# Optimization experiments

Measured on AMD Instinct MI355X. Metric: run time of the kernel, lower is better.

Reference implementation:

```python
import jax, jax.numpy as jnp
import numpy as np

H = 4  # num_heads


def _ln(x, g, b, eps=1e-5):
    m = x.mean(-1, keepdims=True)
    v = ((x - m) ** 2).mean(-1, keepdims=True)
    return (x - m) / jnp.sqrt(v + eps) * g + b


def setup_inputs() -> dict:
    key = jax.random.key(0)
    ks = jax.random.split(key, 16)
    B, N, M, dQ, dK, dV = 4, 2048, 2048, 128, 128, 128
    s = 0.02
    return {
        "Q": jax.random.normal(ks[0], (B, N, dQ), jnp.float32),
        "K": jax.random.normal(ks[1], (B, M, dK), jnp.float32),
        "adj_mask": jax.random.randint(ks[2], (B, N, M), 0, 2, jnp.int32),
        "Wq": jax.random.normal(ks[3], (dQ, dV), jnp.float32) * s,
        "bq": jnp.zeros((dV,), jnp.float32),
        "Wk": jax.random.normal(ks[4], (dK, dV), jnp.float32) * s,
        "bk": jnp.zeros((dV,), jnp.float32),
        "Wv": jax.random.normal(ks[5], (dK, dV), jnp.float32) * s,
        "bv": jnp.zeros((dV,), jnp.float32),
        "Wr1": jax.random.normal(ks[6], (dV, dV), jnp.float32) * s,
        "br1": jnp.zeros((dV,), jnp.float32),
        "Wr2": jax.random.normal(ks[7], (dV, dV), jnp.float32) * s,
        "br2": jnp.zeros((dV,), jnp.float32),
        "g0": jnp.ones((dV,), jnp.float32),
        "be0": jnp.zeros((dV,), jnp.float32),
        "g1": jnp.ones((dV,), jnp.float32),
        "be1": jnp.zeros((dV,), jnp.float32),
    }


def reference(Q, K, adj_mask, Wq, bq, Wk, bk, Wv, bv, Wr1, br1, Wr2, br2, g0, be0, g1, be1):
    B, N, _ = Q.shape
    M = K.shape[1]
    dV = Wq.shape[1]
    dh = dV // H
    Qp = Q @ Wq + bq   # [B,N,dV]
    Kp = K @ Wk + bk   # [B,M,dV]
    Vp = K @ Wv + bv   # [B,M,dV]
    # torch: split dim_V into H chunks, cat along dim 0 -> head-major [H*B, L, dh]
    def to_heads(x, L):
        return x.reshape(B, L, H, dh).transpose(2, 0, 1, 3).reshape(H * B, L, dh)
    Qh, Kh, Vh = to_heads(Qp, N), to_heads(Kp, M), to_heads(Vp, M)
    attn = jnp.einsum('bnd,bmd->bnm', Qh, Kh) / jnp.sqrt(jnp.float32(dh))  # [H*B,N,M]
    # torch repeat_interleave(mask, H, dim=0) gives batch-major order -- faithful
    mask = jnp.repeat(adj_mask, H, axis=0)
    attn = jnp.where(mask == 0, -jnp.inf, attn)
    A = jax.nn.softmax(attn, axis=2)
    O = Qh + jnp.einsum('bnm,bmd->bnd', A, Vh)  # [H*B,N,dh]
    # recombine heads back to [B,N,dV] (intended split(dim=0)/cat(dim=2))
    O = O.reshape(H, B, N, dh).transpose(1, 2, 0, 3).reshape(B, N, dV)
    O = _ln(O, g0, be0)
    O = O + (jax.nn.relu(O @ Wr1 + br1) @ Wr2 + br2)
    return _ln(O, g1, be1)
```

## Files before the change

### kernel.cpp

```cpp
#include <hip/hip_runtime.h>
#include <hip/hip_bf16.h>


typedef short bf16x8 __attribute__((ext_vector_type(8)));
typedef float f32x4 __attribute__((ext_vector_type(4)));

#define BN 4
#define SEQ 2048
#define DIM 128
#define NH 4
#define DH 32
#define ROWS (BN * SEQ)
#define MS 4

static __device__ __forceinline__ unsigned short f2bf(float f) {
    __hip_bfloat16 h = __float2bfloat16(f);
    return *reinterpret_cast<unsigned short*>(&h);
}

__global__ __launch_bounds__(256) void prep_weights(
    const float* __restrict__ Wq, const float* __restrict__ Wk,
    const float* __restrict__ Wv, const float* __restrict__ W1,
    const float* __restrict__ W2, unsigned short* __restrict__ WT)
{
    const float* Ws[5] = {Wq, Wk, Wv, W1, W2};
    const float* W = Ws[blockIdx.x];
    unsigned short* out = WT + blockIdx.x * DIM * DIM;
    for (int i = threadIdx.x; i < DIM * DIM; i += 256) {
        int n = i >> 7, k = i & 127;
        out[i] = f2bf(W[k * DIM + n]);
    }
}

__global__ __launch_bounds__(256) void proj_kernel(
    const float* __restrict__ Q, const float* __restrict__ K,
    const float* __restrict__ bq, const float* __restrict__ bk,
    const float* __restrict__ bv, const unsigned short* __restrict__ WT,
    float* __restrict__ Qp, unsigned short* __restrict__ Qb,
    unsigned short* __restrict__ Kb, unsigned short* __restrict__ Vt)
{
    __shared__ __align__(16) unsigned short sX[64][136];
    __shared__ __align__(16) unsigned short sY[64][137];

    const int proj = blockIdx.y;
    const int rowbase = blockIdx.x * 64;
    const float* X = (proj == 0) ? Q : K;
    const unsigned short* Wt = WT + proj * DIM * DIM;
    const float* bias = (proj == 0) ? bq : (proj == 1) ? bk : bv;

    const int t = threadIdx.x;
    for (int i = 0; i < 8; ++i) {
        int idx = i * 256 + t;
        int row = idx >> 5, c4 = (idx & 31) * 4;
        float4 v = *(const float4*)(X + (rowbase + row) * DIM + c4);
        sX[row][c4 + 0] = f2bf(v.x);
        sX[row][c4 + 1] = f2bf(v.y);
        sX[row][c4 + 2] = f2bf(v.z);
        sX[row][c4 + 3] = f2bf(v.w);
    }
    __syncthreads();

    const int w = t >> 6, lane = t & 63;
    const int n16 = lane & 15, quad = lane >> 4;

    f32x4 acc[4][2];
    for (int r = 0; r < 4; ++r)
        for (int ct = 0; ct < 2; ++ct)
            acc[r][ct] = (f32x4){0.f, 0.f, 0.f, 0.f};

    for (int ks = 0; ks < 4; ++ks) {
        bf16x8 bfrag[2];
        for (int ct = 0; ct < 2; ++ct) {
            int ncol = w * 32 + ct * 16 + n16;
            bfrag[ct] = *(const bf16x8*)(Wt + ncol * DIM + ks * 32 + quad * 8);
        }
        for (int r = 0; r < 4; ++r) {
            bf16x8 afrag = *(const bf16x8*)(&sX[r * 16 + n16][ks * 32 + quad * 8]);
            for (int ct = 0; ct < 2; ++ct)
                acc[r][ct] = __builtin_amdgcn_mfma_f32_16x16x32_bf16(
                    afrag, bfrag[ct], acc[r][ct], 0, 0, 0);
        }
    }

    for (int r = 0; r < 4; ++r) {
        for (int ct = 0; ct < 2; ++ct) {
            int col = w * 32 + ct * 16 + n16;
            float bv_ = bias[col];
            for (int i = 0; i < 4; ++i) {
                int lrow = r * 16 + quad * 4 + i;
                int grow = rowbase + lrow;
                float val = acc[r][ct][i] + bv_;
                if (proj == 0) {
                    Qp[grow * DIM + col] = val;
                    Qb[grow * DIM + col] = f2bf(val * 0.17677669529663687f);
                } else if (proj == 1) {
                    Kb[grow * DIM + col] = f2bf(val);
                } else {
                    sY[lrow][col] = f2bf(val);
                }
            }
        }
    }
    if (proj == 2) {
        __syncthreads();
        int b = rowbase >> 11;
        int mm0 = rowbase & 2047;
        for (int i = 0; i < 32; ++i) {
            int idx = i * 256 + t;
            int c = idx >> 6, m = idx & 63;
            Vt[(b * DIM + c) * SEQ + mm0 + m] = sY[m][c];
        }
    }
}

__global__ __launch_bounds__(256) void attn_kernel(
    const unsigned short* __restrict__ Qb, const unsigned short* __restrict__ Kb,
    const unsigned short* __restrict__ Vt, const int* __restrict__ adj,
    float* __restrict__ Opart, float* __restrict__ Lpart)
{
    __shared__ __align__(16) unsigned short sP[4][16][68];

    const int h = blockIdx.y;
    const int qbase = blockIdx.x * 32;
    const int sp = blockIdx.z;
    const int t = threadIdx.x;
    const int b = t >> 6;
    const int lane = t & 63, n16 = lane & 15, quad = lane >> 4;

    bf16x8 qfrag[2];
#pragma unroll
    for (int r = 0; r < 2; ++r)
        qfrag[r] = *(const bf16x8*)(Qb + ((long)b * SEQ + qbase + r * 16 + n16) * DIM
                                       + h * DH + quad * 8);

    const unsigned short* Kp = Kb + (long)b * SEQ * DIM + h * DH + quad * 8;
    const unsigned short* Vp = Vt + (long)(b * DIM + h * DH) * SEQ + quad * 8;
    const int* Mp = adj + (long)h * SEQ * SEQ + n16;

    int mrow[8];
#pragma unroll
    for (int r = 0; r < 2; ++r)
#pragma unroll
        for (int i = 0; i < 4; ++i)
            mrow[r * 4 + i] = (qbase + r * 16 + quad * 4 + i) * SEQ;

    f32x4 o[2][2];
    float lsum[2][4];
#pragma unroll
    for (int r = 0; r < 2; ++r) {
#pragma unroll
        for (int ct = 0; ct < 2; ++ct) o[r][ct] = (f32x4){0.f, 0.f, 0.f, 0.f};
#pragma unroll
        for (int i = 0; i < 4; ++i) lsum[r][i] = 0.f;
    }

    bf16x8 kf[2][2], vf[2][2];
    int mk[2][16];
    const int mb0 = sp * 512;

#pragma unroll
    for (int c = 0; c < 2; ++c) {
        kf[0][c] = *(const bf16x8*)(Kp + (long)(mb0 + c * 16 + n16) * DIM);
        vf[0][c] = *(const bf16x8*)(Vp + (long)(c * 16 + n16) * SEQ + mb0);
    }
#pragma unroll
    for (int j = 0; j < 8; ++j) {
        mk[0][j]     = Mp[mrow[j] + mb0];
        mk[0][8 + j] = Mp[mrow[j] + mb0 + 16];
    }

    const f32x4 zero4 = {0.f, 0.f, 0.f, 0.f};

#pragma unroll
    for (int mt = 0; mt < 16; ++mt) {
        const int cur = mt & 1, nxt = cur ^ 1;
        if (mt < 15) {
            const int mb = mb0 + (mt + 1) * 32;
#pragma unroll
            for (int c = 0; c < 2; ++c) {
                kf[nxt][c] = *(const bf16x8*)(Kp + (long)(mb + c * 16 + n16) * DIM);
                vf[nxt][c] = *(const bf16x8*)(Vp + (long)(c * 16 + n16) * SEQ + mb);
            }
#pragma unroll
            for (int j = 0; j < 8; ++j) {
                mk[nxt][j]     = Mp[mrow[j] + mb];
                mk[nxt][8 + j] = Mp[mrow[j] + mb + 16];
            }
        }
#pragma unroll
        for (int r = 0; r < 2; ++r) {
            f32x4 s0 = __builtin_amdgcn_mfma_f32_16x16x32_bf16(qfrag[r], kf[cur][0], zero4, 0, 0, 0);
            f32x4 s1 = __builtin_amdgcn_mfma_f32_16x16x32_bf16(qfrag[r], kf[cur][1], zero4, 0, 0, 0);
#pragma unroll
            for (int i = 0; i < 4; ++i) {
                float p0 = mk[cur][r * 4 + i]     ? __expf(s0[i]) : 0.f;
                float p1 = mk[cur][8 + r * 4 + i] ? __expf(s1[i]) : 0.f;
                lsum[r][i] += p0 + p1;
                sP[b][quad * 4 + i][n16]      = f2bf(p0);
                sP[b][quad * 4 + i][16 + n16] = f2bf(p1);
            }
            bf16x8 pa = *(const bf16x8*)(&sP[b][n16][quad * 8]);
#pragma unroll
            for (int ct = 0; ct < 2; ++ct)
                o[r][ct] = __builtin_amdgcn_mfma_f32_16x16x32_bf16(pa, vf[cur][ct], o[r][ct], 0, 0, 0);
        }
    }

#pragma unroll
    for (int d = 1; d < 16; d <<= 1)
#pragma unroll
        for (int r = 0; r < 2; ++r)
#pragma unroll
            for (int i = 0; i < 4; ++i)
                lsum[r][i] += __shfl_xor(lsum[r][i], d, 64);

    float* Ob = Opart + ((long)sp * ROWS + (long)b * SEQ) * DIM;
#pragma unroll
    for (int r = 0; r < 2; ++r)
#pragma unroll
        for (int ct = 0; ct < 2; ++ct)
#pragma unroll
            for (int i = 0; i < 4; ++i)
                Ob[(qbase + r * 16 + quad * 4 + i) * DIM + h * DH + ct * 16 + n16] = o[r][ct][i];

    if (n16 == 0) {
#pragma unroll
        for (int r = 0; r < 2; ++r)
#pragma unroll
            for (int i = 0; i < 4; ++i)
                Lpart[(((long)sp * BN + b) * NH + h) * SEQ + qbase + r * 16 + quad * 4 + i]
                    = lsum[r][i];
    }
}

__global__ __launch_bounds__(256) void epi_kernel(
    const float* __restrict__ Qp, const float* __restrict__ Opart,
    const float* __restrict__ Lpart, const unsigned short* __restrict__ WT,
    const float* __restrict__ br1, const float* __restrict__ br2,
    const float* __restrict__ g0, const float* __restrict__ be0,
    const float* __restrict__ g1, const float* __restrict__ be1,
    float* __restrict__ out)
{
    __shared__ __align__(16) unsigned short sXb[32][136];
    __shared__ __align__(16) unsigned short sHb[32][136];
    __shared__ __align__(16) float sXf[32][132];

    const int rowbase = blockIdx.x * 32;
    const int t = threadIdx.x;
    const int row = t >> 3, c16 = (t & 7) * 16;
    const int grow = rowbase + row;
    const int bidx = grow >> 11;
    const int srow = grow & 2047;
    const int head = c16 >> 5;

    {
        float l = 0.f;
#pragma unroll
        for (int s = 0; s < MS; ++s)
            l += Lpart[(((long)s * BN + bidx) * NH + head) * SEQ + srow];
        float linv = 1.f / l;

        float vals[16];
        float sum = 0.f, ss = 0.f;
#pragma unroll
        for (int j = 0; j < 16; j += 4) {
            float4 qv = *(const float4*)(Qp + (long)grow * DIM + c16 + j);
            float4 ov = {0.f, 0.f, 0.f, 0.f};
#pragma unroll
            for (int s = 0; s < MS; ++s) {
                float4 p = *(const float4*)(Opart + ((long)s * ROWS + grow) * DIM + c16 + j);
                ov.x += p.x; ov.y += p.y; ov.z += p.z; ov.w += p.w;
            }
            vals[j + 0] = qv.x + ov.x * linv;
            vals[j + 1] = qv.y + ov.y * linv;
            vals[j + 2] = qv.z + ov.z * linv;
            vals[j + 3] = qv.w + ov.w * linv;
#pragma unroll
            for (int u = 0; u < 4; ++u) { sum += vals[j + u]; ss += vals[j + u] * vals[j + u]; }
        }
        sum += __shfl_xor(sum, 1, 64); sum += __shfl_xor(sum, 2, 64); sum += __shfl_xor(sum, 4, 64);
        ss  += __shfl_xor(ss, 1, 64);  ss  += __shfl_xor(ss, 2, 64);  ss  += __shfl_xor(ss, 4, 64);
        float mean = sum * (1.f / 128.f);
        float var  = ss * (1.f / 128.f) - mean * mean;
        float rstd = rsqrtf(var + 1e-5f);
#pragma unroll
        for (int j = 0; j < 16; ++j) {
            int col = c16 + j;
            float x = (vals[j] - mean) * rstd * g0[col] + be0[col];
            sXf[row][col] = x;
            sXb[row][col] = f2bf(x);
        }
    }
    __syncthreads();

    const int w = t >> 6, lane = t & 63;
    const int n16 = lane & 15, quad = lane >> 4;
    const unsigned short* W1t = WT + 3 * DIM * DIM;
    const unsigned short* W2t = WT + 4 * DIM * DIM;

    f32x4 acc[2][2];
#pragma unroll
    for (int r = 0; r < 2; ++r)
#pragma unroll
        for (int ct = 0; ct < 2; ++ct) acc[r][ct] = (f32x4){0.f, 0.f, 0.f, 0.f};
    for (int ks = 0; ks < 4; ++ks) {
        bf16x8 bfrag[2];
#pragma unroll
        for (int ct = 0; ct < 2; ++ct)
            bfrag[ct] = *(const bf16x8*)(W1t + (w * 32 + ct * 16 + n16) * DIM + ks * 32 + quad * 8);
#pragma unroll
        for (int r = 0; r < 2; ++r) {
            bf16x8 afrag = *(const bf16x8*)(&sXb[r * 16 + n16][ks * 32 + quad * 8]);
#pragma unroll
            for (int ct = 0; ct < 2; ++ct)
                acc[r][ct] = __builtin_amdgcn_mfma_f32_16x16x32_bf16(
                    afrag, bfrag[ct], acc[r][ct], 0, 0, 0);
        }
    }
#pragma unroll
    for (int r = 0; r < 2; ++r)
#pragma unroll
        for (int ct = 0; ct < 2; ++ct) {
            int col = w * 32 + ct * 16 + n16;
            float bb = br1[col];
#pragma unroll
            for (int i = 0; i < 4; ++i) {
                float hv = acc[r][ct][i] + bb;
                sHb[r * 16 + quad * 4 + i][col] = f2bf(fmaxf(hv, 0.f));
            }
        }
    __syncthreads();

    f32x4 acc2[2][2];
#pragma unroll
    for (int r = 0; r < 2; ++r)
#pragma unroll
        for (int ct = 0; ct < 2; ++ct) acc2[r][ct] = (f32x4){0.f, 0.f, 0.f, 0.f};
    for (int ks = 0; ks < 4; ++ks) {
        bf16x8 bfrag[2];
#pragma unroll
        for (int ct = 0; ct < 2; ++ct)
            bfrag[ct] = *(const bf16x8*)(W2t + (w * 32 + ct * 16 + n16) * DIM + ks * 32 + quad * 8);
#pragma unroll
        for (int r = 0; r < 2; ++r) {
            bf16x8 afrag = *(const bf16x8*)(&sHb[r * 16 + n16][ks * 32 + quad * 8]);
#pragma unroll
            for (int ct = 0; ct < 2; ++ct)
                acc2[r][ct] = __builtin_amdgcn_mfma_f32_16x16x32_bf16(
                    afrag, bfrag[ct], acc2[r][ct], 0, 0, 0);
        }
    }
    float yv[2][2][4];
#pragma unroll
    for (int r = 0; r < 2; ++r)
#pragma unroll
        for (int ct = 0; ct < 2; ++ct) {
            int col = w * 32 + ct * 16 + n16;
            float bb = br2[col];
#pragma unroll
            for (int i = 0; i < 4; ++i)
                yv[r][ct][i] = acc2[r][ct][i] + bb + sXf[r * 16 + quad * 4 + i][col];
        }
    __syncthreads();
#pragma unroll
    for (int r = 0; r < 2; ++r)
#pragma unroll
        for (int ct = 0; ct < 2; ++ct) {
            int col = w * 32 + ct * 16 + n16;
#pragma unroll
            for (int i = 0; i < 4; ++i)
                sXf[r * 16 + quad * 4 + i][col] = yv[r][ct][i];
        }
    __syncthreads();

    {
        float vals[16];
        float sum = 0.f, ss = 0.f;
#pragma unroll
        for (int j = 0; j < 16; ++j) {
            float v = sXf[row][c16 + j];
            vals[j] = v; sum += v; ss += v * v;
        }
        sum += __shfl_xor(sum, 1, 64); sum += __shfl_xor(sum, 2, 64); sum += __shfl_xor(sum, 4, 64);
        ss  += __shfl_xor(ss, 1, 64);  ss  += __shfl_xor(ss, 2, 64);  ss  += __shfl_xor(ss, 4, 64);
        float mean = sum * (1.f / 128.f);
        float var  = ss * (1.f / 128.f) - mean * mean;
        float rstd = rsqrtf(var + 1e-5f);
        float* op = out + (long)grow * DIM + c16;
#pragma unroll
        for (int j = 0; j < 16; j += 4) {
            float4 ov;
            int col = c16 + j;
            ov.x = (vals[j + 0] - mean) * rstd * g1[col + 0] + be1[col + 0];
            ov.y = (vals[j + 1] - mean) * rstd * g1[col + 1] + be1[col + 1];
            ov.z = (vals[j + 2] - mean) * rstd * g1[col + 2] + be1[col + 2];
            ov.w = (vals[j + 3] - mean) * rstd * g1[col + 3] + be1[col + 3];
            *(float4*)(op + j) = ov;
        }
    }
}

extern "C" void kernel_launch(void* const* d_in, const int* in_sizes, int n_in,
                              void* d_out, int out_size, void* d_ws, size_t ws_size,
                              hipStream_t stream) {
    const float* Q   = (const float*)d_in[0];
    const float* K   = (const float*)d_in[1];
    const int*   adj = (const int*)d_in[2];
    const float* Wq  = (const float*)d_in[3];
    const float* bq  = (const float*)d_in[4];
    const float* Wk  = (const float*)d_in[5];
    const float* bk  = (const float*)d_in[6];
    const float* Wv  = (const float*)d_in[7];
    const float* bv  = (const float*)d_in[8];
    const float* Wr1 = (const float*)d_in[9];
    const float* br1 = (const float*)d_in[10];
    const float* Wr2 = (const float*)d_in[11];
    const float* br2 = (const float*)d_in[12];
    const float* g0  = (const float*)d_in[13];
    const float* be0 = (const float*)d_in[14];
    const float* g1  = (const float*)d_in[15];
    const float* be1 = (const float*)d_in[16];
    float* out = (float*)d_out;

    float* Qp          = (float*)d_ws;
    float* Opart       = Qp + (long)ROWS * DIM;
    float* Lpart       = Opart + (long)MS * ROWS * DIM;
    unsigned short* Qb = (unsigned short*)(Lpart + (long)MS * BN * NH * SEQ);
    unsigned short* Kb = Qb + (long)ROWS * DIM;
    unsigned short* Vt = Kb + (long)ROWS * DIM;
    unsigned short* WT = Vt + (long)ROWS * DIM;

    prep_weights<<<5, 256, 0, stream>>>(Wq, Wk, Wv, Wr1, Wr2, WT);
    proj_kernel<<<dim3(128, 3), 256, 0, stream>>>(Q, K, bq, bk, bv, WT,
                                                  Qp, Qb, Kb, Vt);
    attn_kernel<<<dim3(64, NH, MS), 256, 0, stream>>>(Qb, Kb, Vt, adj, Opart, Lpart);
    epi_kernel<<<256, 256, 0, stream>>>(Qp, Opart, Lpart, WT, br1, br2,
                                        g0, be0, g1, be1, out);
}
```

Measured before the change: 188.6 us.

## Bit-pack adjacency mask, store bf16 partial outputs, shrink proj/epilogue tiles

A new prep kernel packs the int32 adjacency mask into 32-bit words before the attention kernel runs, so attention reads one bit per key instead of a full int32. Partial attention outputs are now stored as bf16 instead of fp32, which halves the traffic between the attention and epilogue kernels at some cost in precision. The projection and epilogue kernels use half the rows per block to launch more blocks. The attention inner loop is also reordered so all four QK MFMAs issue before the softmax and P writes.

```diff
diff --git a/kernel.cpp b/kernel.cpp
--- a/kernel.cpp
+++ b/kernel.cpp
@@ -12,24 +12,48 @@
 #define DH 32
 #define ROWS (BN * SEQ)
 #define MS 4
+#define MWORDS (SEQ / 32)
 
 static __device__ __forceinline__ unsigned short f2bf(float f) {
     __hip_bfloat16 h = __float2bfloat16(f);
     return *reinterpret_cast<unsigned short*>(&h);
 }
-
-__global__ __launch_bounds__(256) void prep_weights(
+static __device__ __forceinline__ float bf2f(unsigned short u) {
+    union { unsigned int i; float f; } cv;
+    cv.i = ((unsigned int)u) << 16;
+    return cv.f;
+}
+
+__global__ __launch_bounds__(256) void pack_prep(
+    const int* __restrict__ adj,
     const float* __restrict__ Wq, const float* __restrict__ Wk,
     const float* __restrict__ Wv, const float* __restrict__ W1,
-    const float* __restrict__ W2, unsigned short* __restrict__ WT)
+    const float* __restrict__ W2,
+    unsigned int* __restrict__ bits, unsigned short* __restrict__ WT)
 {
-    const float* Ws[5] = {Wq, Wk, Wv, W1, W2};
-    const float* W = Ws[blockIdx.x];
-    unsigned short* out = WT + blockIdx.x * DIM * DIM;
-    for (int i = threadIdx.x; i < DIM * DIM; i += 256) {
-        int n = i >> 7, k = i & 127;
-        out[i] = f2bf(W[k * DIM + n]);
-    }
+    const int bx = blockIdx.x;
+    if (bx >= 2048) {
+        const float* Ws[5] = {Wq, Wk, Wv, W1, W2};
+        const float* W = Ws[bx - 2048];
+        unsigned short* out = WT + (bx - 2048) * DIM * DIM;
+        for (int i = threadIdx.x; i < DIM * DIM; i += 256) {
+            int n = i >> 7, k = i & 127;
+            out[i] = f2bf(W[k * DIM + n]);
+        }
+        return;
+    }
+    const int wid = bx * 256 + threadIdx.x;
+    const int4* src = (const int4*)(adj + (long)wid * 32);
+    unsigned int w = 0;
+#pragma unroll
+    for (int j = 0; j < 8; ++j) {
+        int4 v = src[j];
+        w |= (((unsigned)v.x & 1u) << (4 * j))
+           | (((unsigned)v.y & 1u) << (4 * j + 1))
+           | (((unsigned)v.z & 1u) << (4 * j + 2))
+           | (((unsigned)v.w & 1u) << (4 * j + 3));
+    }
+    bits[wid] = w;
 }
 
 __global__ __launch_bounds__(256) void proj_kernel(
@@ -39,20 +63,21 @@
     float* __restrict__ Qp, unsigned short* __restrict__ Qb,
     unsigned short* __restrict__ Kb, unsigned short* __restrict__ Vt)
 {
-    __shared__ __align__(16) unsigned short sX[64][136];
-    __shared__ __align__(16) unsigned short sY[64][137];
+    __shared__ __align__(16) unsigned short sX[32][136];
+    __shared__ __align__(16) unsigned short sY[32][137];
 
     const int proj = blockIdx.y;
-    const int rowbase = blockIdx.x * 64;
+    const int rowbase = blockIdx.x * 32;
     const float* X = (proj == 0) ? Q : K;
     const unsigned short* Wt = WT + proj * DIM * DIM;
     const float* bias = (proj == 0) ? bq : (proj == 1) ? bk : bv;
 
     const int t = threadIdx.x;
-    for (int i = 0; i < 8; ++i) {
+#pragma unroll
+    for (int i = 0; i < 4; ++i) {
         int idx = i * 256 + t;
         int row = idx >> 5, c4 = (idx & 31) * 4;
-        float4 v = *(const float4*)(X + (rowbase + row) * DIM + c4);
+        float4 v = *(const float4*)(X + (long)(rowbase + row) * DIM + c4);
         sX[row][c4 + 0] = f2bf(v.x);
         sX[row][c4 + 1] = f2bf(v.y);
         sX[row][c4 + 2] = f2bf(v.z);
@@ -63,38 +88,46 @@
     const int w = t >> 6, lane = t & 63;
     const int n16 = lane & 15, quad = lane >> 4;
 
-    f32x4 acc[4][2];
-    for (int r = 0; r < 4; ++r)
+    f32x4 acc[2][2];
+#pragma unroll
+    for (int r = 0; r < 2; ++r)
+#pragma unroll
         for (int ct = 0; ct < 2; ++ct)
             acc[r][ct] = (f32x4){0.f, 0.f, 0.f, 0.f};
 
     for (int ks = 0; ks < 4; ++ks) {
         bf16x8 bfrag[2];
+#pragma unroll
         for (int ct = 0; ct < 2; ++ct) {
             int ncol = w * 32 + ct * 16 + n16;
             bfrag[ct] = *(const bf16x8*)(Wt + ncol * DIM + ks * 32 + quad * 8);
         }
-        for (int r = 0; r < 4; ++r) {
+#pragma unroll
+        for (int r = 0; r < 2; ++r) {
             bf16x8 afrag = *(const bf16x8*)(&sX[r * 16 + n16][ks * 32 + quad * 8]);
+#pragma unroll
             for (int ct = 0; ct < 2; ++ct)
                 acc[r][ct] = __builtin_amdgcn_mfma_f32_16x16x32_bf16(
                     afrag, bfrag[ct], acc[r][ct], 0, 0, 0);
         }
     }
 
-    for (int r = 0; r < 4; ++r) {
+#pragma unroll
+    for (int r = 0; r < 2; ++r) {
+#pragma unroll
         for (int ct = 0; ct < 2; ++ct) {
             int col = w * 32 + ct * 16 + n16;
             float bv_ = bias[col];
+#pragma unroll
             for (int i = 0; i < 4; ++i) {
                 int lrow = r * 16 + quad * 4 + i;
                 int grow = rowbase + lrow;
                 float val = acc[r][ct][i] + bv_;
                 if (proj == 0) {
-                    Qp[grow * DIM + col] = val;
-                    Qb[grow * DIM + col] = f2bf(val * 0.17677669529663687f);
+                    Qp[(long)grow * DIM + col] = val;
+                    Qb[(long)grow * DIM + col] = f2bf(val * 0.17677669529663687f);
                 } else if (proj == 1) {
-                    Kb[grow * DIM + col] = f2bf(val);
+                    Kb[(long)grow * DIM + col] = f2bf(val);
                 } else {
                     sY[lrow][col] = f2bf(val);
                 }
@@ -105,20 +138,21 @@
         __syncthreads();
         int b = rowbase >> 11;
         int mm0 = rowbase & 2047;
-        for (int i = 0; i < 32; ++i) {
+#pragma unroll
+        for (int i = 0; i < 16; ++i) {
             int idx = i * 256 + t;
-            int c = idx >> 6, m = idx & 63;
-            Vt[(b * DIM + c) * SEQ + mm0 + m] = sY[m][c];
+            int c = idx >> 5, m = idx & 31;
+            Vt[((long)b * DIM + c) * SEQ + mm0 + m] = sY[m][c];
         }
     }
 }
 
 __global__ __launch_bounds__(256) void attn_kernel(
     const unsigned short* __restrict__ Qb, const unsigned short* __restrict__ Kb,
-    const unsigned short* __restrict__ Vt, const int* __restrict__ adj,
-    float* __restrict__ Opart, float* __restrict__ Lpart)
+    const unsigned short* __restrict__ Vt, const unsigned int* __restrict__ mbits,
+    unsigned short* __restrict__ Opart, float* __restrict__ Lpart)
 {
-    __shared__ __align__(16) unsigned short sP[4][16][68];
+    __shared__ __align__(16) unsigned short sP[4][32][68];
 
     const int h = blockIdx.y;
     const int qbase = blockIdx.x * 32;
@@ -135,14 +169,14 @@
 
     const unsigned short* Kp = Kb + (long)b * SEQ * DIM + h * DH + quad * 8;
     const unsigned short* Vp = Vt + (long)(b * DIM + h * DH) * SEQ + quad * 8;
-    const int* Mp = adj + (long)h * SEQ * SEQ + n16;
-
-    int mrow[8];
+
+    int mrowb[8];
 #pragma unroll
     for (int r = 0; r < 2; ++r)
 #pragma unroll
         for (int i = 0; i < 4; ++i)
-            mrow[r * 4 + i] = (qbase + r * 16 + quad * 4 + i) * SEQ;
+            mrowb[r * 4 + i] = (h * SEQ + qbase + r * 16 + quad * 4 + i) * MWORDS
+                             + sp * 16;
 
     f32x4 o[2][2];
     float lsum[2][4];
@@ -155,7 +189,7 @@
     }
 
     bf16x8 kf[2][2], vf[2][2];
-    int mk[2][16];
+    unsigned int mk[2][8];
     const int mb0 = sp * 512;
 
 #pragma unroll
@@ -164,10 +198,7 @@
         vf[0][c] = *(const bf16x8*)(Vp + (long)(c * 16 + n16) * SEQ + mb0);
     }
 #pragma unroll
-    for (int j = 0; j < 8; ++j) {
-        mk[0][j]     = Mp[mrow[j] + mb0];
-        mk[0][8 + j] = Mp[mrow[j] + mb0 + 16];
-    }
+    for (int j = 0; j < 8; ++j) mk[0][j] = mbits[mrowb[j]];
 
     const f32x4 zero4 = {0.f, 0.f, 0.f, 0.f};
 
@@ -182,27 +213,33 @@
                 vf[nxt][c] = *(const bf16x8*)(Vp + (long)(c * 16 + n16) * SEQ + mb);
             }
 #pragma unroll
-            for (int j = 0; j < 8; ++j) {
-                mk[nxt][j]     = Mp[mrow[j] + mb];
-                mk[nxt][8 + j] = Mp[mrow[j] + mb + 16];
+            for (int j = 0; j < 8; ++j) mk[nxt][j] = mbits[mrowb[j] + mt + 1];
+        }
+        f32x4 s[2][2];
+#pragma unroll
+        for (int r = 0; r < 2; ++r)
+#pragma unroll
+            for (int c = 0; c < 2; ++c)
+                s[r][c] = __builtin_amdgcn_mfma_f32_16x16x32_bf16(
+                    qfrag[r], kf[cur][c], zero4, 0, 0, 0);
+#pragma unroll
+        for (int r = 0; r < 2; ++r)
+#pragma unroll
+            for (int i = 0; i < 4; ++i) {
+                unsigned int w = mk[cur][r * 4 + i];
+                float p0 = ((w >> n16) & 1u)        ? __expf(s[r][0][i]) : 0.f;
+                float p1 = ((w >> (16 + n16)) & 1u) ? __expf(s[r][1][i]) : 0.f;
+                lsum[r][i] += p0 + p1;
+                sP[b][r * 16 + quad * 4 + i][n16]      = f2bf(p0);
+                sP[b][r * 16 + quad * 4 + i][16 + n16] = f2bf(p1);
             }
-        }
 #pragma unroll
         for (int r = 0; r < 2; ++r) {
-            f32x4 s0 = __builtin_amdgcn_mfma_f32_16x16x32_bf16(qfrag[r], kf[cur][0], zero4, 0, 0, 0);
-            f32x4 s1 = __builtin_amdgcn_mfma_f32_16x16x32_bf16(qfrag[r], kf[cur][1], zero4, 0, 0, 0);
-#pragma unroll
-            for (int i = 0; i < 4; ++i) {
-                float p0 = mk[cur][r * 4 + i]     ? __expf(s0[i]) : 0.f;
-                float p1 = mk[cur][8 + r * 4 + i] ? __expf(s1[i]) : 0.f;
-                lsum[r][i] += p0 + p1;
-                sP[b][quad * 4 + i][n16]      = f2bf(p0);
-                sP[b][quad * 4 + i][16 + n16] = f2bf(p1);
-            }
-            bf16x8 pa = *(const bf16x8*)(&sP[b][n16][quad * 8]);
+            bf16x8 pa = *(const bf16x8*)(&sP[b][r * 16 + n16][quad * 8]);
 #pragma unroll
             for (int ct = 0; ct < 2; ++ct)
-                o[r][ct] = __builtin_amdgcn_mfma_f32_16x16x32_bf16(pa, vf[cur][ct], o[r][ct], 0, 0, 0);
+                o[r][ct] = __builtin_amdgcn_mfma_f32_16x16x32_bf16(
+                    pa, vf[cur][ct], o[r][ct], 0, 0, 0);
         }
     }
 
@@ -214,14 +251,15 @@
             for (int i = 0; i < 4; ++i)
                 lsum[r][i] += __shfl_xor(lsum[r][i], d, 64);
 
-    float* Ob = Opart + ((long)sp * ROWS + (long)b * SEQ) * DIM;
+    unsigned short* Ob = Opart + ((long)sp * ROWS + (long)b * SEQ) * DIM;
 #pragma unroll
     for (int r = 0; r < 2; ++r)
 #pragma unroll
         for (int ct = 0; ct < 2; ++ct)
 #pragma unroll
             for (int i = 0; i < 4; ++i)
-                Ob[(qbase + r * 16 + quad * 4 + i) * DIM + h * DH + ct * 16 + n16] = o[r][ct][i];
+                Ob[(long)(qbase + r * 16 + quad * 4 + i) * DIM + h * DH + ct * 16 + n16]
+                    = f2bf(o[r][ct][i]);
 
     if (n16 == 0) {
 #pragma unroll
@@ -234,24 +272,24 @@
 }
 
 __global__ __launch_bounds__(256) void epi_kernel(
-    const float* __restrict__ Qp, const float* __restrict__ Opart,
+    const float* __restrict__ Qp, const unsigned short* __restrict__ Opart,
     const float* __restrict__ Lpart, const unsigned short* __restrict__ WT,
     const float* __restrict__ br1, const float* __restrict__ br2,
     const float* __restrict__ g0, const float* __restrict__ be0,
     const float* __restrict__ g1, const float* __restrict__ be1,
     float* __restrict__ out)
 {
-    __shared__ __align__(16) unsigned short sXb[32][136];
-    __shared__ __align__(16) unsigned short sHb[32][136];
-    __shared__ __align__(16) float sXf[32][132];
-
-    const int rowbase = blockIdx.x * 32;
+    __shared__ __align__(16) unsigned short sXb[16][136];
+    __shared__ __align__(16) unsigned short sHb[16][136];
+    __shared__ __align__(16) float sXf[16][132];
+
+    const int rowbase = blockIdx.x * 16;
     const int t = threadIdx.x;
-    const int row = t >> 3, c16 = (t & 7) * 16;
+    const int row = t >> 4, col8 = (t & 15) * 8;
     const int grow = rowbase + row;
     const int bidx = grow >> 11;
     const int srow = grow & 2047;
-    const int head = c16 >> 5;
+    const int head = col8 >> 5;
 
     {
         float l = 0.f;
@@ -260,32 +298,38 @@
             l += Lpart[(((long)s * BN + bidx) * NH + head) * SEQ + srow];
         float linv = 1.f / l;
 
-        float vals[16];
+        float ovf[8];
+#pragma unroll
+        for (int j = 0; j < 8; ++j) ovf[j] = 0.f;
+#pragma unroll
+        for (int s = 0; s < MS; ++s) {
+            bf16x8 p = *(const bf16x8*)(Opart + ((long)s * ROWS + grow) * DIM + col8);
+#pragma unroll
+            for (int j = 0; j < 8; ++j) ovf[j] += bf2f((unsigned short)p[j]);
+        }
+
+        float vals[8];
         float sum = 0.f, ss = 0.f;
 #pragma unroll
-        for (int j = 0; j < 16; j += 4) {
-            float4 qv = *(const float4*)(Qp + (long)grow * DIM + c16 + j);
-            float4 ov = {0.f, 0.f, 0.f, 0.f};
-#pragma unroll
-            for (int s = 0; s < MS; ++s) {
-                float4 p = *(const float4*)(Opart + ((long)s * ROWS + grow) * DIM + c16 + j);
-                ov.x += p.x; ov.y += p.y; ov.z += p.z; ov.w += p.w;
-            }
-            vals[j + 0] = qv.x + ov.x * linv;
-            vals[j + 1] = qv.y + ov.y * linv;
-            vals[j + 2] = qv.z + ov.z * linv;
-            vals[j + 3] = qv.w + ov.w * linv;
+        for (int j = 0; j < 8; j += 4) {
+            float4 qv = *(const float4*)(Qp + (long)grow * DIM + col8 + j);
+            vals[j + 0] = qv.x + ovf[j + 0] * linv;
+            vals[j + 1] = qv.y + ovf[j + 1] * linv;
+            vals[j + 2] = qv.z + ovf[j + 2] * linv;
+            vals[j + 3] = qv.w + ovf[j + 3] * linv;
 #pragma unroll
             for (int u = 0; u < 4; ++u) { sum += vals[j + u]; ss += vals[j + u] * vals[j + u]; }
         }
-        sum += __shfl_xor(sum, 1, 64); sum += __shfl_xor(sum, 2, 64); sum += __shfl_xor(sum, 4, 64);
-        ss  += __shfl_xor(ss, 1, 64);  ss  += __shfl_xor(ss, 2, 64);  ss  += __shfl_xor(ss, 4, 64);
+        sum += __shfl_xor(sum, 1, 64); sum += __shfl_xor(sum, 2, 64);
+        sum += __shfl_xor(sum, 4, 64); sum += __shfl_xor(sum, 8, 64);
+        ss  += __shfl_xor(ss, 1, 64);  ss  += __shfl_xor(ss, 2, 64);
+        ss  += __shfl_xor(ss, 4, 64);  ss  += __shfl_xor(ss, 8, 64);
         float mean = sum * (1.f / 128.f);
         float var  = ss * (1.f / 128.f) - mean * mean;
         float rstd = rsqrtf(var + 1e-5f);
 #pragma unroll
-        for (int j = 0; j < 16; ++j) {
-            int col = c16 + j;
+        for (int j = 0; j < 8; ++j) {
+            int col = col8 + j;
             float x = (vals[j] - mean) * rstd * g0[col] + be0[col];
             sXf[row][col] = x;
             sXb[row][col] = f2bf(x);
@@ -298,99 +342,79 @@
     const unsigned short* W1t = WT + 3 * DIM * DIM;
     const unsigned short* W2t = WT + 4 * DIM * DIM;
 
-    f32x4 acc[2][2];
-#pragma unroll
-    for (int r = 0; r < 2; ++r)
-#pragma unroll
-        for (int ct = 0; ct < 2; ++ct) acc[r][ct] = (f32x4){0.f, 0.f, 0.f, 0.f};
+    f32x4 acc[2];
+#pragma unroll
+    for (int ct = 0; ct < 2; ++ct) acc[ct] = (f32x4){0.f, 0.f, 0.f, 0.f};
     for (int ks = 0; ks < 4; ++ks) {
-        bf16x8 bfrag[2];
-#pragma unroll
-        for (int ct = 0; ct < 2; ++ct)
-            bfrag[ct] = *(const bf16x8*)(W1t + (w * 32 + ct * 16 + n16) * DIM + ks * 32 + quad * 8);
-#pragma unroll
-        for (int r = 0; r < 2; ++r) {
-            bf16x8 afrag = *(const bf16x8*)(&sXb[r * 16 + n16][ks * 32 + quad * 8]);
-#pragma unroll
-            for (int ct = 0; ct < 2; ++ct)
-                acc[r][ct] = __builtin_amdgcn_mfma_f32_16x16x32_bf16(
-                    afrag, bfrag[ct], acc[r][ct], 0, 0, 0);
-        }
-    }
-#pragma unroll
-    for (int r = 0; r < 2; ++r)
+        bf16x8 afrag = *(const bf16x8*)(&sXb[n16][ks * 32 + quad * 8]);
 #pragma unroll
         for (int ct = 0; ct < 2; ++ct) {
-            int col = w * 32 + ct * 16 + n16;
-            float bb = br1[col];
-#pragma unroll
-            for (int i = 0; i < 4; ++i) {
-                float hv = acc[r][ct][i] + bb;
-                sHb[r * 16 + quad * 4 + i][col] = f2bf(fmaxf(hv, 0.f));
-            }
-        }
+            bf16x8 bfrag = *(const bf16x8*)(W1t + (w * 32 + ct * 16 + n16) * DIM + ks * 32 + quad * 8);
+            acc[ct] = __builtin_amdgcn_mfma_f32_16x16x32_bf16(afrag, bfrag, acc[ct], 0, 0, 0);
+        }
+    }
+#pragma unroll
+    for (int ct = 0; ct < 2; ++ct) {
+        int col = w * 32 + ct * 16 + n16;
+        float bb = br1[col];
+#pragma unroll
+        for (int i = 0; i < 4; ++i) {
+            float hv = acc[ct][i] + bb;
+            sHb[quad * 4 + i][col] = f2bf(fmaxf(hv, 0.f));
+        }
+    }
     __syncthreads();
 
-    f32x4 acc2[2][2];
-#pragma unroll
-    for (int r = 0; r < 2; ++r)
-#pragma unroll
-        for (int ct = 0; ct < 2; ++ct) acc2[r][ct] = (f32x4){0.f, 0.f, 0.f, 0.f};
+    f32x4 acc2[2];
+#pragma unroll
+    for (int ct = 0; ct < 2; ++ct) acc2[ct] = (f32x4){0.f, 0.f, 0.f, 0.f};
     for (int ks = 0; ks < 4; ++ks) {
-        bf16x8 bfrag[2];
-#pragma unroll
-        for (int ct = 0; ct < 2; ++ct)
-            bfrag[ct] = *(const bf16x8*)(W2t + (w * 32 + ct * 16 + n16) * DIM + ks * 32 + quad * 8);
-#pragma unroll
-        for (int r = 0; r < 2; ++r) {
-            bf16x8 afrag = *(const bf16x8*)(&sHb[r * 16 + n16][ks * 32 + quad * 8]);
-#pragma unroll
-            for (int ct = 0; ct < 2; ++ct)
-                acc2[r][ct] = __builtin_amdgcn_mfma_f32_16x16x32_bf16(
-                    afrag, bfrag[ct], acc2[r][ct], 0, 0, 0);
-        }
-    }
-    float yv[2][2][4];
-#pragma unroll
-    for (int r = 0; r < 2; ++r)
+        bf16x8 afrag = *(const bf16x8*)(&sHb[n16][ks * 32 + quad * 8]);
 #pragma unroll
         for (int ct = 0; ct < 2; ++ct) {
-            int col = w * 32 + ct * 16 + n16;
-            float bb = br2[col];
-#pragma unroll
-            for (int i = 0; i < 4; ++i)
-                yv[r][ct][i] = acc2[r][ct][i] + bb + sXf[r * 16 + quad * 4 + i][col];
-        }
+            bf16x8 bfrag = *(const bf16x8*)(W2t + (w * 32 + ct * 16 + n16) * DIM + ks * 32 + quad * 8);
+            acc2[ct] = __builtin_amdgcn_mfma_f32_16x16x32_bf16(afrag, bfrag, acc2[ct], 0, 0, 0);
+        }
+    }
+    float yv[2][4];
+#pragma unroll
+    for (int ct = 0; ct < 2; ++ct) {
+        int col = w * 32 + ct * 16 + n16;
+        float bb = br2[col];
+#pragma unroll
+        for (int i = 0; i < 4; ++i)
+            yv[ct][i] = acc2[ct][i] + bb + sXf[quad * 4 + i][col];
+    }
     __syncthreads();
 #pragma unroll
-    for (int r = 0; r < 2; ++r)
-#pragma unroll
-        for (int ct = 0; ct < 2; ++ct) {
-            int col = w * 32 + ct * 16 + n16;
-#pragma unroll
-            for (int i = 0; i < 4; ++i)
-                sXf[r * 16 + quad * 4 + i][col] = yv[r][ct][i];
-        }
+    for (int ct = 0; ct < 2; ++ct) {
+        int col = w * 32 + ct * 16 + n16;
+#pragma unroll
+        for (int i = 0; i < 4; ++i)
+            sXf[quad * 4 + i][col] = yv[ct][i];
+    }
     __syncthreads();
 
     {
-        float vals[16];
+        float vals[8];
         float sum = 0.f, ss = 0.f;
 #pragma unroll
-        for (int j = 0; j < 16; ++j) {
-            float v = sXf[row][c16 + j];
+        for (int j = 0; j < 8; ++j) {
+            float v = sXf[row][col8 + j];
             vals[j] = v; sum += v; ss += v * v;
         }
-        sum += __shfl_xor(sum, 1, 64); sum += __shfl_xor(sum, 2, 64); sum += __shfl_xor(sum, 4, 64);
-        ss  += __shfl_xor(ss, 1, 64);  ss  += __shfl_xor(ss, 2, 64);  ss  += __shfl_xor(ss, 4, 64);
+        sum += __shfl_xor(sum, 1, 64); sum += __shfl_xor(sum, 2, 64);
+        sum += __shfl_xor(sum, 4, 64); sum += __shfl_xor(sum, 8, 64);
+        ss  += __shfl_xor(ss, 1, 64);  ss  += __shfl_xor(ss, 2, 64);
+        ss  += __shfl_xor(ss, 4, 64);  ss  += __shfl_xor(ss, 8, 64);
         float mean = sum * (1.f / 128.f);
         float var  = ss * (1.f / 128.f) - mean * mean;
         float rstd = rsqrtf(var + 1e-5f);
-        float* op = out + (long)grow * DIM + c16;
-#pragma unroll
-        for (int j = 0; j < 16; j += 4) {
+        float* op = out + (long)grow * DIM + col8;
+#pragma unroll
+        for (int j = 0; j < 8; j += 4) {
             float4 ov;
-            int col = c16 + j;
+            int col = col8 + j;
             ov.x = (vals[j + 0] - mean) * rstd * g1[col + 0] + be1[col + 0];
             ov.y = (vals[j + 1] - mean) * rstd * g1[col + 1] + be1[col + 1];
             ov.z = (vals[j + 2] - mean) * rstd * g1[col + 2] + be1[col + 2];
@@ -422,18 +446,19 @@
     const float* be1 = (const float*)d_in[16];
     float* out = (float*)d_out;
 
-    float* Qp          = (float*)d_ws;
-    float* Opart       = Qp + (long)ROWS * DIM;
-    float* Lpart       = Opart + (long)MS * ROWS * DIM;
-    unsigned short* Qb = (unsigned short*)(Lpart + (long)MS * BN * NH * SEQ);
-    unsigned short* Kb = Qb + (long)ROWS * DIM;
-    unsigned short* Vt = Kb + (long)ROWS * DIM;
-    unsigned short* WT = Vt + (long)ROWS * DIM;
-
-    prep_weights<<<5, 256, 0, stream>>>(Wq, Wk, Wv, Wr1, Wr2, WT);
-    proj_kernel<<<dim3(128, 3), 256, 0, stream>>>(Q, K, bq, bk, bv, WT,
+    float* Qp             = (float*)d_ws;
+    unsigned short* Opart = (unsigned short*)(Qp + (long)ROWS * DIM);
+    float* Lpart          = (float*)(Opart + (long)MS * ROWS * DIM);
+    unsigned short* Qb    = (unsigned short*)(Lpart + (long)MS * BN * NH * SEQ);
+    unsigned short* Kb    = Qb + (long)ROWS * DIM;
+    unsigned short* Vt    = Kb + (long)ROWS * DIM;
+    unsigned short* WT    = Vt + (long)ROWS * DIM;
+    unsigned int*   bits  = (unsigned int*)(WT + 5 * DIM * DIM);
+
+    pack_prep<<<2053, 256, 0, stream>>>(adj, Wq, Wk, Wv, Wr1, Wr2, bits, WT);
+    proj_kernel<<<dim3(256, 3), 256, 0, stream>>>(Q, K, bq, bk, bv, WT,
                                                   Qp, Qb, Kb, Vt);
-    attn_kernel<<<dim3(64, NH, MS), 256, 0, stream>>>(Qb, Kb, Vt, adj, Opart, Lpart);
-    epi_kernel<<<256, 256, 0, stream>>>(Qp, Opart, Lpart, WT, br1, br2,
+    attn_kernel<<<dim3(64, NH, MS), 256, 0, stream>>>(Qb, Kb, Vt, bits, Opart, Lpart);
+    epi_kernel<<<512, 256, 0, stream>>>(Qp, Opart, Lpart, WT, br1, br2,
                                         g0, be0, g1, be1, out);
 }
```

Measured after the change: 221.8 us. +17.6%, slower.
